# Kernel tuning notes

Hardware: AMD Instinct MI355X
Metric: run time of the kernel (lower is better)

## Reference

```python
import jax, jax.numpy as jnp
import numpy as np

N, IN_CH, OUT_CH = 2, 16, 32
SPATIAL = (20, 20, 20, 20)
KER = (3, 3, 3, 3)


def setup_inputs() -> dict:
    key = jax.random.key(0)
    kx, kw = jax.random.split(key)
    x = jax.random.normal(kx, (N, IN_CH) + SPATIAL, dtype=jnp.float32)
    # kaiming-uniform-like init scale; exact init distribution irrelevant for correctness baseline
    fan_in = IN_CH * int(np.prod(KER))
    bound = float(np.sqrt(6.0 / fan_in))
    w = jax.random.uniform(kw, (IN_CH, OUT_CH) + KER, dtype=jnp.float32,
                           minval=-bound, maxval=bound)
    return {"x": x, "w": w}


def reference(x, w):
    # x: [n, in_ch, d1, d2, d3, d4]; w: [in_ch, out_ch, k1, k2, k3, k4]
    # valid 4D convolution (cross-correlation), stride 1 -- same math as the
    # torch as_strided im2col + tensordot, but expressed as a sum over the
    # (small, fixed) kernel offsets to avoid materializing the im2col tensor.
    kd = w.shape[2:]
    od = tuple(x.shape[2 + i] - kd[i] + 1 for i in range(4))  # output spatial dims
    out = jnp.zeros((x.shape[0], w.shape[1]) + od, dtype=x.dtype)
    for a in range(kd[0]):
        for b in range(kd[1]):
            for c in range(kd[2]):
                for d in range(kd[3]):
                    patch = x[:, :, a:a + od[0], b:b + od[1], c:c + od[2], d:d + od[3]]
                    out = out + jnp.einsum('ncijkl,co->noijkl', patch, w[:, :, a, b, c, d])
    return out
```

## Files before the change

### kernel.cpp

```cpp
#include <hip/hip_runtime.h>


typedef unsigned short ushort_t;
typedef __attribute__((ext_vector_type(8)))  __bf16 bf16x8;
typedef __attribute__((ext_vector_type(16))) float  f32x16;
typedef __attribute__((ext_vector_type(4)))  unsigned int uint4v;

__device__ __forceinline__ ushort_t f2bf(float f) {
    union { float f; unsigned int u; } v; v.f = f;
    unsigned int r = v.u + 0x7FFFu + ((v.u >> 16) & 1u);
    return (ushort_t)(r >> 16);
}

__global__ __launch_bounds__(256) void prepass(const float* __restrict__ x,
                                               const float* __restrict__ w,
                                               ushort_t* __restrict__ xt,
                                               ushort_t* __restrict__ wt) {
    const int blk = blockIdx.x;
    if (blk < 1250) {
        const int g = blk * 256 + threadIdx.x;
        const int n = g / 160000, rem = g % 160000;
        const float* xs = x + (size_t)n * 2560000 + rem;
        unsigned int pk[8];
        #pragma unroll
        for (int e = 0; e < 8; ++e) {
            unsigned int lo = f2bf(xs[(size_t)(2 * e) * 160000]);
            unsigned int hi = f2bf(xs[(size_t)(2 * e + 1) * 160000]);
            pk[e] = lo | (hi << 16);
        }
        uint4v* q = (uint4v*)xt + (size_t)g * 2;
        uint4v q0; q0[0] = pk[0]; q0[1] = pk[1]; q0[2] = pk[2]; q0[3] = pk[3];
        uint4v q1; q1[0] = pk[4]; q1[1] = pk[5]; q1[2] = pk[6]; q1[3] = pk[7];
        q[0] = q0; q[1] = q1;
    } else {
        const int s = (blk - 1250) * 256 + threadIdx.x;
        if (s < 41472) {
            const int ic = s / 2592, rem = s % 2592;
            const int oc = rem / 81, tap = rem % 81;
            wt[tap * 512 + oc * 16 + ic] = f2bf(w[s]);
        }
    }
}

__global__ __launch_bounds__(256, 2) void conv4d_mfma(
    const ushort_t* __restrict__ xt, const ushort_t* __restrict__ wt,
    float* __restrict__ out)
{
    __shared__ float edge[384];

    const int wgid = blockIdx.x;
    const int tile_ = (wgid & 7) * 81 + (wgid >> 3);
    const int n = tile_ / 324;
    const int rem_ = tile_ - n * 324;
    const int j = rem_ / 18, i = rem_ % 18;

    const int t = threadIdx.x;
    const int lane = t & 63, wv = t >> 6;
    const int col = lane & 31, ic8 = lane >> 5;

    int sp[3]; int cb[3];
    #pragma unroll
    for (int m = 0; m < 3; ++m) {
        sp[m] = (3 * wv + m) * 32 + col;
        const int spc = sp[m] > 359 ? 359 : sp[m];
        cb[m] = spc * 32 + ic8 * 16;
    }

    f32x16 acc[3][3];
    #pragma unroll
    for (int d = 0; d < 3; ++d)
        #pragma unroll
        for (int m = 0; m < 3; ++m)
            #pragma unroll
            for (int r = 0; r < 16; ++r) acc[d][m][r] = 0.0f;

    const char* xnij = (const char*)(xt + (size_t)n * 2560000
                                        + (size_t)i * 128000 + (size_t)j * 6400);

    #pragma unroll 3
    for (int ab = 0; ab < 9; ++ab) {
        const int a = ab / 3, b = ab % 3;
        const char* xs = xnij + ((size_t)a * 128000 + (size_t)b * 6400) * 2;
        const ushort_t* wtb = wt + (size_t)ab * 4608 + col * 16 + ic8 * 8;
        #pragma unroll
        for (int c = 0; c < 3; ++c) {
            bf16x8 af0 = *(const bf16x8*)(wtb + (c * 3 + 0) * 512);
            bf16x8 af1 = *(const bf16x8*)(wtb + (c * 3 + 1) * 512);
            bf16x8 af2 = *(const bf16x8*)(wtb + (c * 3 + 2) * 512);
            #pragma unroll
            for (int m = 0; m < 3; ++m) {
                bf16x8 bv = *(const bf16x8*)(xs + cb[m] + c * 640);
                acc[0][m] = __builtin_amdgcn_mfma_f32_32x32x16_bf16(af0, bv, acc[0][m], 0, 0, 0);
                acc[1][m] = __builtin_amdgcn_mfma_f32_32x32x16_bf16(af1, bv, acc[1][m], 0, 0, 0);
                acc[2][m] = __builtin_amdgcn_mfma_f32_32x32x16_bf16(af2, bv, acc[2][m], 0, 0, 0);
            }
        }
    }

    if (col == 0) {
        #pragma unroll
        for (int r = 0; r < 16; ++r) {
            edge[((wv * 3 + 0) * 2 + ic8) * 16 + r] = acc[1][0][r];
            edge[((wv * 3 + 1) * 2 + ic8) * 16 + r] = acc[2][0][r];
        }
    } else if (col == 1) {
        #pragma unroll
        for (int r = 0; r < 16; ++r)
            edge[((wv * 3 + 2) * 2 + ic8) * 16 + r] = acc[2][0][r];
    }
    __syncthreads();
    const int nw = wv < 3 ? wv + 1 : 3;

    bool valm[3]; float* po[3];
    float* outn = out + (size_t)n * 3359232 + (size_t)i * 5832 + (size_t)j * 324
                      + (size_t)ic8 * 419904;
    #pragma unroll
    for (int m = 0; m < 3; ++m) {
        const int s = sp[m];
        const int k = s / 20, ls = s % 20;
        valm[m] = (ls <= 17) && (s <= 357);
        po[m] = outn + k * 18 + ls;
    }
    const int src1 = (lane & 32) | ((col + 1) & 31);
    const int src2 = (lane & 32) | ((col + 2) & 31);

    #pragma unroll
    for (int r = 0; r < 16; ++r) {
        const float e1  = edge[((nw * 3 + 0) * 2 + ic8) * 16 + r];
        const float e2a = edge[((nw * 3 + 1) * 2 + ic8) * 16 + r];
        const float e2b = edge[((nw * 3 + 2) * 2 + ic8) * 16 + r];
        float t1[4], t2[4];
        #pragma unroll
        for (int m = 0; m < 3; ++m) {
            t1[m] = __shfl(acc[1][m][r], src1, 64);
            t2[m] = __shfl(acc[2][m][r], src2, 64);
        }
        t1[3] = e1;
        t2[3] = (col == 30) ? e2a : e2b;
        const int offr = ((r & 3) + 8 * (r >> 2)) * 104976;
        #pragma unroll
        for (int m = 0; m < 3; ++m) {
            const float v1m = (col == 31) ? t1[m + 1] : t1[m];
            const float v2m = (col >= 30) ? t2[m + 1] : t2[m];
            const float res = acc[0][m][r] + v1m + v2m;
            if (valm[m]) po[m][offr] = res;
        }
    }
}

extern "C" void kernel_launch(void* const* d_in, const int* in_sizes, int n_in,
                              void* d_out, int out_size, void* d_ws, size_t ws_size,
                              hipStream_t stream) {
    const float* x = (const float*)d_in[0];
    const float* w = (const float*)d_in[1];
    float* out = (float*)d_out;

    ushort_t* xt = (ushort_t*)d_ws;
    ushort_t* wt = (ushort_t*)((char*)d_ws + (size_t)10240000);

    prepass<<<dim3(1412), 256, 0, stream>>>(x, w, xt, wt);
    conv4d_mfma<<<dim3(648), 256, 0, stream>>>(xt, wt, out);
}
```

Measured before the change: 49.66 us.

## Split conv tiles into overlapping 30-wide wave strips to drop LDS edge exchange

Each workgroup now covers a third of the (i,j) plane slice. Every wave handles one 32-column strip that starts 30 positions after the previous one, so the two halo columns needed by the d-offset shifts are recomputed in place instead of being exchanged through shared memory with a barrier. The grid triples to 1944 workgroups, per-thread accumulators shrink from nine to three MFMA tiles, and launch bounds rise to 4 waves per SIMD to raise occupancy. In exchange each wave does about 7% redundant MFMA work on the overlapping columns, and weight fragments are reloaded across more workgroups.

```diff
diff --git a/kernel.cpp b/kernel.cpp
--- a/kernel.cpp
+++ b/kernel.cpp
@@ -42,37 +42,30 @@
     }
 }
 
-__global__ __launch_bounds__(256, 2) void conv4d_mfma(
+__global__ __launch_bounds__(256, 4) void conv4d_mfma(
     const ushort_t* __restrict__ xt, const ushort_t* __restrict__ wt,
     float* __restrict__ out)
 {
-    __shared__ float edge[384];
-
     const int wgid = blockIdx.x;
-    const int tile_ = (wgid & 7) * 81 + (wgid >> 3);
-    const int n = tile_ / 324;
-    const int rem_ = tile_ - n * 324;
-    const int j = rem_ / 18, i = rem_ % 18;
+    const int g = (wgid & 7) * 243 + (wgid >> 3);
+    const int n = g / 972;
+    int rem = g - n * 972;
+    const int j = rem / 54;  rem -= j * 54;
+    const int i = rem / 3;
+    const int q = rem - i * 3;
 
     const int t = threadIdx.x;
     const int lane = t & 63, wv = t >> 6;
     const int col = lane & 31, ic8 = lane >> 5;
 
-    int sp[3]; int cb[3];
+    const int T = q * 4 + wv;
+    const int sp = T * 30 + col;
+    const int spc = sp > 359 ? 359 : sp;
+    const int cb = spc * 32 + ic8 * 16;
+
+    f32x16 acc0, acc1, acc2;
     #pragma unroll
-    for (int m = 0; m < 3; ++m) {
-        sp[m] = (3 * wv + m) * 32 + col;
-        const int spc = sp[m] > 359 ? 359 : sp[m];
-        cb[m] = spc * 32 + ic8 * 16;
-    }
-
-    f32x16 acc[3][3];
-    #pragma unroll
-    for (int d = 0; d < 3; ++d)
-        #pragma unroll
-        for (int m = 0; m < 3; ++m)
-            #pragma unroll
-            for (int r = 0; r < 16; ++r) acc[d][m][r] = 0.0f;
+    for (int r = 0; r < 16; ++r) { acc0[r] = 0.0f; acc1[r] = 0.0f; acc2[r] = 0.0f; }
 
     const char* xnij = (const char*)(xt + (size_t)n * 2560000
                                         + (size_t)i * 128000 + (size_t)j * 6400);
@@ -87,64 +80,28 @@
             bf16x8 af0 = *(const bf16x8*)(wtb + (c * 3 + 0) * 512);
             bf16x8 af1 = *(const bf16x8*)(wtb + (c * 3 + 1) * 512);
             bf16x8 af2 = *(const bf16x8*)(wtb + (c * 3 + 2) * 512);
-            #pragma unroll
-            for (int m = 0; m < 3; ++m) {
-                bf16x8 bv = *(const bf16x8*)(xs + cb[m] + c * 640);
-                acc[0][m] = __builtin_amdgcn_mfma_f32_32x32x16_bf16(af0, bv, acc[0][m], 0, 0, 0);
-                acc[1][m] = __builtin_amdgcn_mfma_f32_32x32x16_bf16(af1, bv, acc[1][m], 0, 0, 0);
-                acc[2][m] = __builtin_amdgcn_mfma_f32_32x32x16_bf16(af2, bv, acc[2][m], 0, 0, 0);
-            }
+            bf16x8 bv  = *(const bf16x8*)(xs + cb + c * 640);
+            acc0 = __builtin_amdgcn_mfma_f32_32x32x16_bf16(af0, bv, acc0, 0, 0, 0);
+            acc1 = __builtin_amdgcn_mfma_f32_32x32x16_bf16(af1, bv, acc1, 0, 0, 0);
+            acc2 = __builtin_amdgcn_mfma_f32_32x32x16_bf16(af2, bv, acc2, 0, 0, 0);
         }
     }
 
-    if (col == 0) {
-        #pragma unroll
-        for (int r = 0; r < 16; ++r) {
-            edge[((wv * 3 + 0) * 2 + ic8) * 16 + r] = acc[1][0][r];
-            edge[((wv * 3 + 1) * 2 + ic8) * 16 + r] = acc[2][0][r];
-        }
-    } else if (col == 1) {
-        #pragma unroll
-        for (int r = 0; r < 16; ++r)
-            edge[((wv * 3 + 2) * 2 + ic8) * 16 + r] = acc[2][0][r];
-    }
-    __syncthreads();
-    const int nw = wv < 3 ? wv + 1 : 3;
-
-    bool valm[3]; float* po[3];
-    float* outn = out + (size_t)n * 3359232 + (size_t)i * 5832 + (size_t)j * 324
-                      + (size_t)ic8 * 419904;
-    #pragma unroll
-    for (int m = 0; m < 3; ++m) {
-        const int s = sp[m];
-        const int k = s / 20, ls = s % 20;
-        valm[m] = (ls <= 17) && (s <= 357);
-        po[m] = outn + k * 18 + ls;
-    }
+    const int s = sp;
+    const int k = s / 20, ls = s % 20;
+    const bool val = (col <= 29) && (ls <= 17) && (s <= 357);
+    float* po = out + (size_t)n * 3359232 + (size_t)i * 5832 + (size_t)j * 324
+                    + (size_t)ic8 * 419904 + k * 18 + ls;
     const int src1 = (lane & 32) | ((col + 1) & 31);
     const int src2 = (lane & 32) | ((col + 2) & 31);
 
     #pragma unroll
     for (int r = 0; r < 16; ++r) {
-        const float e1  = edge[((nw * 3 + 0) * 2 + ic8) * 16 + r];
-        const float e2a = edge[((nw * 3 + 1) * 2 + ic8) * 16 + r];
-        const float e2b = edge[((nw * 3 + 2) * 2 + ic8) * 16 + r];
-        float t1[4], t2[4];
-        #pragma unroll
-        for (int m = 0; m < 3; ++m) {
-            t1[m] = __shfl(acc[1][m][r], src1, 64);
-            t2[m] = __shfl(acc[2][m][r], src2, 64);
-        }
-        t1[3] = e1;
-        t2[3] = (col == 30) ? e2a : e2b;
+        const float v1 = __shfl(acc1[r], src1, 64);
+        const float v2 = __shfl(acc2[r], src2, 64);
+        const float res = acc0[r] + v1 + v2;
         const int offr = ((r & 3) + 8 * (r >> 2)) * 104976;
-        #pragma unroll
-        for (int m = 0; m < 3; ++m) {
-            const float v1m = (col == 31) ? t1[m + 1] : t1[m];
-            const float v2m = (col >= 30) ? t2[m + 1] : t2[m];
-            const float res = acc[0][m][r] + v1m + v2m;
-            if (valm[m]) po[m][offr] = res;
-        }
+        if (val) po[offr] = res;
     }
 }
 
@@ -159,5 +116,5 @@
     ushort_t* wt = (ushort_t*)((char*)d_ws + (size_t)10240000);
 
     prepass<<<dim3(1412), 256, 0, stream>>>(x, w, xt, wt);
-    conv4d_mfma<<<dim3(648), 256, 0, stream>>>(xt, wt, out);
+    conv4d_mfma<<<dim3(1944), 256, 0, stream>>>(xt, wt, out);
 }
```

After: 46.45 us. -6.5%, faster.
